# Kernel optimization log

Measured on AMD Instinct MI355X. Metric: run time of the kernel, lower is better.

Reference implementation:

```python
import jax, jax.numpy as jnp
import numpy as np

GRID_SIZE = 16
NUM_VOXELS = GRID_SIZE ** 3


def setup_inputs() -> dict:
    key = jax.random.key(0)
    k1, k2, k3 = jax.random.split(key, 3)
    B, D, N = 4, 128, 100000
    features = jax.random.normal(k1, (B, D, N), dtype=jnp.float32)
    xyz_normalized = jax.random.uniform(k2, (B, N, 3), dtype=jnp.float32)
    mask = jax.random.randint(k3, (B, N), 0, 2, dtype=jnp.int32)
    return {"features": features, "xyz_normalized": xyz_normalized, "mask": mask}


def _flat_voxel_idx(xyz):
    # xyz: [B, N, 3] in [0,1); voxel index per point, flattened z*G*G + y*G + x
    G = GRID_SIZE
    vi = jnp.clip((xyz * G).astype(jnp.int32), 0, G - 1)  # [B, N, 3]
    return vi[..., 2] * (G * G) + vi[..., 1] * G + vi[..., 0]  # [B, N]


def reference(features, xyz_normalized, mask):
    # features: [B, D, N], xyz_normalized: [B, N, 3], mask: [B, N] int (0/1)
    idx = _flat_voxel_idx(xyz_normalized)  # [B, N]
    feats = features * mask[:, None, :].astype(features.dtype)  # [B, D, N]

    def per_batch(f_dn, idx_n, m_n):
        # scatter-add features: segment_sum over points -> [V, D] -> [D, V]
        sums = jax.ops.segment_sum(f_dn.T, idx_n, num_segments=NUM_VOXELS)  # [V, D]
        counts = jax.ops.segment_sum(m_n, idx_n, num_segments=NUM_VOXELS)  # [V]
        counts = jnp.maximum(counts, 1).astype(f_dn.dtype)
        return (sums / counts[:, None]).T  # [D, V]

    return jax.vmap(per_batch)(feats, idx, mask)  # [B, D, V]
```

## Files before the change

kernel.cpp:

```cpp
#include <hip/hip_runtime.h>

#define GSZ  16
#define NVOX 4096
#define BB   4
#define DD   128

__global__ void k_voxidx(const float* __restrict__ xyz, const int* __restrict__ mask,
                         unsigned short* __restrict__ idxm, int* __restrict__ counts,
                         int N) {
    int n = blockIdx.x * blockDim.x + threadIdx.x;
    int b = blockIdx.y;
    if (n >= N) return;
    size_t i = (size_t)b * N + n;
    float x = xyz[3 * i + 0];
    float y = xyz[3 * i + 1];
    float z = xyz[3 * i + 2];
    int vx = min(max((int)(x * (float)GSZ), 0), GSZ - 1);
    int vy = min(max((int)(y * (float)GSZ), 0), GSZ - 1);
    int vz = min(max((int)(z * (float)GSZ), 0), GSZ - 1);
    int idx = vz * GSZ * GSZ + vy * GSZ + vx;
    if (mask[i] != 0) {
        idxm[i] = (unsigned short)idx;
        atomicAdd(&counts[b * NVOX + idx], 1);
    } else {
        idxm[i] = 0xFFFFu;
    }
}

__global__ __launch_bounds__(1024, 8) void k_scatter(const float* __restrict__ feats,
                                                     const unsigned short* __restrict__ idxm,
                                                     const int* __restrict__ counts,
                                                     float* __restrict__ out, int N) {
    __shared__ float acc[NVOX];
    int d = blockIdx.x & (DD - 1);
    int b = blockIdx.x >> 7;

    for (int j = threadIdx.x; j < NVOX; j += 1024) acc[j] = 0.f;
    __syncthreads();

    const float*          f  = feats + ((size_t)b * DD + (size_t)d) * (size_t)N;
    const unsigned short* ib = idxm + (size_t)b * N;

    const int stride = 1024 * 8;
    const int nmain  = (N / stride) * stride;
    const int niter  = nmain / stride;
    const int t8     = (int)threadIdx.x * 8;

#define PROC(id, val)                                        \
    {                                                        \
        unsigned int _i = (id);                              \
        if (_i != 0xFFFFu) atomicAdd(&acc[_i], (val));       \
    }

    if (niter > 0) {
        uint4  iv = *reinterpret_cast<const uint4*>(ib + t8);
        float4 r0 = *reinterpret_cast<const float4*>(f + t8);
        float4 r1 = *reinterpret_cast<const float4*>(f + t8 + 4);
        for (int it = 0; it < niter; it++) {
            int inext = (it + 1 < niter) ? (it + 1) * stride + t8 : t8;
            uint4  ivn = *reinterpret_cast<const uint4*>(ib + inext);
            float4 r0n = *reinterpret_cast<const float4*>(f + inext);
            float4 r1n = *reinterpret_cast<const float4*>(f + inext + 4);

            PROC(iv.x & 0xFFFFu, r0.x)
            PROC(iv.x >> 16,     r0.y)
            PROC(iv.y & 0xFFFFu, r0.z)
            PROC(iv.y >> 16,     r0.w)
            PROC(iv.z & 0xFFFFu, r1.x)
            PROC(iv.z >> 16,     r1.y)
            PROC(iv.w & 0xFFFFu, r1.z)
            PROC(iv.w >> 16,     r1.w)

            iv = ivn; r0 = r0n; r1 = r1n;
        }
    }
    for (int p = nmain + (int)threadIdx.x; p < N; p += 1024) {
        unsigned int id = ib[p];
        if (id != 0xFFFFu) atomicAdd(&acc[id], f[p]);
    }
#undef PROC

    __syncthreads();

    const int* cb = counts + b * NVOX;
    float*     ob = out + ((size_t)b * DD + (size_t)d) * (size_t)NVOX;
    {
        int j = threadIdx.x;
        float4 a = reinterpret_cast<float4*>(acc)[j];
        int4   c = reinterpret_cast<const int4*>(cb)[j];
        a.x /= (float)max(c.x, 1);
        a.y /= (float)max(c.y, 1);
        a.z /= (float)max(c.z, 1);
        a.w /= (float)max(c.w, 1);
        reinterpret_cast<float4*>(ob)[j] = a;
    }
}

extern "C" void kernel_launch(void* const* d_in, const int* in_sizes, int n_in,
                              void* d_out, int out_size, void* d_ws, size_t ws_size,
                              hipStream_t stream) {
    const float* feats = (const float*)d_in[0];
    const float* xyz   = (const float*)d_in[1];
    const int*   mask  = (const int*)d_in[2];
    float*       out   = (float*)d_out;

    int N = in_sizes[2] / BB;

    int*            counts = (int*)d_ws;
    unsigned short* idxm   = (unsigned short*)((char*)d_ws +
                                               (size_t)BB * NVOX * sizeof(int));

    hipMemsetAsync(counts, 0, (size_t)BB * NVOX * sizeof(int), stream);

    k_voxidx<<<dim3((N + 255) / 256, BB), 256, 0, stream>>>(xyz, mask, idxm, counts, N);

    k_scatter<<<BB * DD, 1024, 0, stream>>>(feats, idxm, counts, out, N);
}
```

Measured before the change: 350.4 us.

## Compact masked points before scatter to skip masked-out work

Adds a stream-compaction pipeline: the voxel-index pass packs each point's position and voxel id into one 32-bit word and counts valid points per tile, a scan kernel computes tile offsets, and a compact kernel writes only unmasked entries. The scatter kernel then iterates only over valid points, gathering features by index instead of streaming all features contiguously. This is meant to halve the atomics and the loop trip count, at the cost of extra kernels and uncoalesced gathers of the feature rows. The gather still pulls whole cache lines, so feature bandwidth may not shrink much.

```diff
diff --git a/kernel.cpp b/kernel.cpp
--- a/kernel.cpp
+++ b/kernel.cpp
@@ -4,31 +4,139 @@
 #define NVOX 4096
 #define BB   4
 #define DD   128
-
-__global__ void k_voxidx(const float* __restrict__ xyz, const int* __restrict__ mask,
-                         unsigned short* __restrict__ idxm, int* __restrict__ counts,
-                         int N) {
-    int n = blockIdx.x * blockDim.x + threadIdx.x;
-    int b = blockIdx.y;
-    if (n >= N) return;
-    size_t i = (size_t)b * N + n;
-    float x = xyz[3 * i + 0];
-    float y = xyz[3 * i + 1];
-    float z = xyz[3 * i + 2];
-    int vx = min(max((int)(x * (float)GSZ), 0), GSZ - 1);
-    int vy = min(max((int)(y * (float)GSZ), 0), GSZ - 1);
-    int vz = min(max((int)(z * (float)GSZ), 0), GSZ - 1);
-    int idx = vz * GSZ * GSZ + vy * GSZ + vx;
-    if (mask[i] != 0) {
-        idxm[i] = (unsigned short)idx;
-        atomicAdd(&counts[b * NVOX + idx], 1);
+#define TPB1 256
+#define TILE 2048
+#define PPT  8
+
+__global__ __launch_bounds__(TPB1) void k_voxidx(const float* __restrict__ xyz,
+                                                 const int* __restrict__ mask,
+                                                 unsigned int* __restrict__ pack,
+                                                 int* __restrict__ counts,
+                                                 int* __restrict__ bcount,
+                                                 int N, int NB) {
+    int tile = blockIdx.x, b = blockIdx.y;
+    __shared__ int s_cnt;
+    if (threadIdx.x == 0) s_cnt = 0;
+    __syncthreads();
+
+    const float*  xb = xyz  + (size_t)b * N * 3;
+    const int*    mb = mask + (size_t)b * N;
+    unsigned int* pb = pack + (size_t)b * N;
+    int*          cb = counts + b * NVOX;
+
+    int p0 = tile * TILE + (int)threadIdx.x * PPT;
+    int cnt = 0;
+
+    if (p0 + PPT <= N) {
+        float a[3 * PPT];
+        float4* av = (float4*)a;
+        const float4* xv = (const float4*)(xb + 3 * (size_t)p0);
+#pragma unroll
+        for (int q = 0; q < 6; q++) av[q] = xv[q];
+        const int4* mv = (const int4*)(mb + p0);
+        int4 mA = mv[0], mB = mv[1];
+        int mk[PPT] = {mA.x, mA.y, mA.z, mA.w, mB.x, mB.y, mB.z, mB.w};
+        unsigned int pk[PPT];
+#pragma unroll
+        for (int k = 0; k < PPT; k++) {
+            int vx = min(max((int)(a[3 * k + 0] * (float)GSZ), 0), GSZ - 1);
+            int vy = min(max((int)(a[3 * k + 1] * (float)GSZ), 0), GSZ - 1);
+            int vz = min(max((int)(a[3 * k + 2] * (float)GSZ), 0), GSZ - 1);
+            int idx = vz * GSZ * GSZ + vy * GSZ + vx;
+            if (mk[k] != 0) {
+                pk[k] = ((unsigned int)(p0 + k) << 12) | (unsigned int)idx;
+                cnt++;
+                atomicAdd(&cb[idx], 1);
+            } else {
+                pk[k] = 0xFFFFFFFFu;
+            }
+        }
+        uint4* pv = (uint4*)(pb + p0);
+        pv[0] = make_uint4(pk[0], pk[1], pk[2], pk[3]);
+        pv[1] = make_uint4(pk[4], pk[5], pk[6], pk[7]);
     } else {
-        idxm[i] = 0xFFFFu;
+        for (int k = 0; k < PPT; k++) {
+            int p = p0 + k;
+            if (p >= N) break;
+            float x = xb[3 * (size_t)p + 0];
+            float y = xb[3 * (size_t)p + 1];
+            float z = xb[3 * (size_t)p + 2];
+            int vx = min(max((int)(x * (float)GSZ), 0), GSZ - 1);
+            int vy = min(max((int)(y * (float)GSZ), 0), GSZ - 1);
+            int vz = min(max((int)(z * (float)GSZ), 0), GSZ - 1);
+            int idx = vz * GSZ * GSZ + vy * GSZ + vx;
+            if (mb[p] != 0) {
+                pb[p] = ((unsigned int)p << 12) | (unsigned int)idx;
+                cnt++;
+                atomicAdd(&cb[idx], 1);
+            } else {
+                pb[p] = 0xFFFFFFFFu;
+            }
+        }
+    }
+    atomicAdd(&s_cnt, cnt);
+    __syncthreads();
+    if (threadIdx.x == 0) bcount[b * NB + tile] = s_cnt;
+}
+
+__global__ void k_scan(const int* __restrict__ bcount, int* __restrict__ boff,
+                       int* __restrict__ M, int NB) {
+    int b = threadIdx.x;
+    if (b < BB) {
+        int run = 0;
+        for (int j = 0; j < NB; j++) {
+            boff[b * NB + j] = run;
+            run += bcount[b * NB + j];
+        }
+        M[b] = run;
+    }
+}
+
+__global__ __launch_bounds__(TPB1) void k_compact(const unsigned int* __restrict__ pack,
+                                                  const int* __restrict__ boff,
+                                                  unsigned int* __restrict__ comp,
+                                                  int N, int NB) {
+    int tile = blockIdx.x, b = blockIdx.y;
+    const unsigned int* pb = pack + (size_t)b * N;
+    unsigned int*       ob = comp + (size_t)b * N;
+
+    int p0 = tile * TILE + (int)threadIdx.x * PPT;
+    unsigned int pk[PPT];
+#pragma unroll
+    for (int k = 0; k < PPT; k++) pk[k] = 0xFFFFFFFFu;
+
+    if (p0 + PPT <= N) {
+        const uint4* pv = (const uint4*)(pb + p0);
+        uint4 A = pv[0], Bq = pv[1];
+        pk[0] = A.x;  pk[1] = A.y;  pk[2] = A.z;  pk[3] = A.w;
+        pk[4] = Bq.x; pk[5] = Bq.y; pk[6] = Bq.z; pk[7] = Bq.w;
+    } else {
+        for (int k = 0; k < PPT; k++)
+            if (p0 + k < N) pk[k] = pb[p0 + k];
+    }
+    int cnt = 0;
+#pragma unroll
+    for (int k = 0; k < PPT; k++) cnt += (pk[k] != 0xFFFFFFFFu) ? 1 : 0;
+
+    __shared__ int s[TPB1];
+    s[threadIdx.x] = cnt;
+    __syncthreads();
+    for (int off = 1; off < TPB1; off <<= 1) {
+        int v = (threadIdx.x >= (unsigned)off) ? s[threadIdx.x - off] : 0;
+        __syncthreads();
+        s[threadIdx.x] += v;
+        __syncthreads();
+    }
+    int pos = boff[b * NB + tile] + s[threadIdx.x] - cnt;
+#pragma unroll
+    for (int k = 0; k < PPT; k++) {
+        if (pk[k] != 0xFFFFFFFFu) ob[pos++] = pk[k];
     }
 }
 
 __global__ __launch_bounds__(1024, 8) void k_scatter(const float* __restrict__ feats,
-                                                     const unsigned short* __restrict__ idxm,
+                                                     const unsigned int* __restrict__ comp,
+                                                     const int* __restrict__ M,
                                                      const int* __restrict__ counts,
                                                      float* __restrict__ out, int N) {
     __shared__ float acc[NVOX];
@@ -38,48 +146,35 @@
     for (int j = threadIdx.x; j < NVOX; j += 1024) acc[j] = 0.f;
     __syncthreads();
 
-    const float*          f  = feats + ((size_t)b * DD + (size_t)d) * (size_t)N;
-    const unsigned short* ib = idxm + (size_t)b * N;
-
-    const int stride = 1024 * 8;
-    const int nmain  = (N / stride) * stride;
-    const int niter  = nmain / stride;
-    const int t8     = (int)threadIdx.x * 8;
-
-#define PROC(id, val)                                        \
-    {                                                        \
-        unsigned int _i = (id);                              \
-        if (_i != 0xFFFFu) atomicAdd(&acc[_i], (val));       \
-    }
+    int Mb = M[b];
+    const float*        f  = feats + ((size_t)b * DD + (size_t)d) * (size_t)N;
+    const unsigned int* cp = comp + (size_t)b * N;
+
+    const int stride = 1024 * 4;
+    int niter = Mb / stride;
+    int nmain = niter * stride;
+    int t4 = (int)threadIdx.x * 4;
 
     if (niter > 0) {
-        uint4  iv = *reinterpret_cast<const uint4*>(ib + t8);
-        float4 r0 = *reinterpret_cast<const float4*>(f + t8);
-        float4 r1 = *reinterpret_cast<const float4*>(f + t8 + 4);
+        uint4 e = *reinterpret_cast<const uint4*>(cp + t4);
         for (int it = 0; it < niter; it++) {
-            int inext = (it + 1 < niter) ? (it + 1) * stride + t8 : t8;
-            uint4  ivn = *reinterpret_cast<const uint4*>(ib + inext);
-            float4 r0n = *reinterpret_cast<const float4*>(f + inext);
-            float4 r1n = *reinterpret_cast<const float4*>(f + inext + 4);
-
-            PROC(iv.x & 0xFFFFu, r0.x)
-            PROC(iv.x >> 16,     r0.y)
-            PROC(iv.y & 0xFFFFu, r0.z)
-            PROC(iv.y >> 16,     r0.w)
-            PROC(iv.z & 0xFFFFu, r1.x)
-            PROC(iv.z >> 16,     r1.y)
-            PROC(iv.w & 0xFFFFu, r1.z)
-            PROC(iv.w >> 16,     r1.w)
-
-            iv = ivn; r0 = r0n; r1 = r1n;
-        }
-    }
-    for (int p = nmain + (int)threadIdx.x; p < N; p += 1024) {
-        unsigned int id = ib[p];
-        if (id != 0xFFFFu) atomicAdd(&acc[id], f[p]);
-    }
-#undef PROC
-
+            int inext = (it + 1 < niter) ? (it + 1) * stride + t4 : t4;
+            uint4 en = *reinterpret_cast<const uint4*>(cp + inext);
+            float v0 = f[e.x >> 12];
+            float v1 = f[e.y >> 12];
+            float v2 = f[e.z >> 12];
+            float v3 = f[e.w >> 12];
+            atomicAdd(&acc[e.x & 0xFFFu], v0);
+            atomicAdd(&acc[e.y & 0xFFFu], v1);
+            atomicAdd(&acc[e.z & 0xFFFu], v2);
+            atomicAdd(&acc[e.w & 0xFFFu], v3);
+            e = en;
+        }
+    }
+    for (int p = nmain + (int)threadIdx.x; p < Mb; p += 1024) {
+        unsigned int ee = cp[p];
+        atomicAdd(&acc[ee & 0xFFFu], f[ee >> 12]);
+    }
     __syncthreads();
 
     const int* cb = counts + b * NVOX;
@@ -104,15 +199,21 @@
     const int*   mask  = (const int*)d_in[2];
     float*       out   = (float*)d_out;
 
-    int N = in_sizes[2] / BB;
-
-    int*            counts = (int*)d_ws;
-    unsigned short* idxm   = (unsigned short*)((char*)d_ws +
-                                               (size_t)BB * NVOX * sizeof(int));
+    int N  = in_sizes[2] / BB;
+    int NB = (N + TILE - 1) / TILE;
+
+    char* w = (char*)d_ws;
+    int*          counts = (int*)w;                       w += (size_t)BB * NVOX * sizeof(int);
+    int*          bcount = (int*)w;                       w += ((size_t)BB * NB * sizeof(int) + 255) & ~255ull;
+    int*          boff   = (int*)w;                       w += ((size_t)BB * NB * sizeof(int) + 255) & ~255ull;
+    int*          Mcnt   = (int*)w;                       w += 256;
+    unsigned int* pack   = (unsigned int*)w;              w += (size_t)BB * N * sizeof(unsigned int);
+    unsigned int* comp   = (unsigned int*)w;
 
     hipMemsetAsync(counts, 0, (size_t)BB * NVOX * sizeof(int), stream);
 
-    k_voxidx<<<dim3((N + 255) / 256, BB), 256, 0, stream>>>(xyz, mask, idxm, counts, N);
-
-    k_scatter<<<BB * DD, 1024, 0, stream>>>(feats, idxm, counts, out, N);
-}
+    k_voxidx <<<dim3(NB, BB), TPB1, 0, stream>>>(xyz, mask, pack, counts, bcount, N, NB);
+    k_scan   <<<1, 64, 0, stream>>>(bcount, boff, Mcnt, NB);
+    k_compact<<<dim3(NB, BB), TPB1, 0, stream>>>(pack, boff, comp, N, NB);
+    k_scatter<<<BB * DD, 1024, 0, stream>>>(feats, comp, Mcnt, counts, out, N);
+}
```

After: 361.9 us. 1.03x slower.

## Accumulate two channels per LDS atomic using packed fp16 adds, per-tile histograms

Applied to the files above, without the earlier changes.

The scatter kernel now handles two feature channels per block. Both values for a point are packed into one fp16x2 and added with a single ds_pk_add_f16 LDS atomic, which halves the number of shared-memory atomics and blocks. The global count atomics and the memset are replaced by per-tile LDS histograms written out as ushort, and the scatter kernel reduces them. The prep kernel now handles 16 points per thread with vectorized loads. The cost is that voxel sums are accumulated in fp16, which loses accuracy and may exceed tolerance.

```diff
diff --git a/kernel.cpp b/kernel.cpp
--- a/kernel.cpp
+++ b/kernel.cpp
@@ -1,99 +1,172 @@
 #include <hip/hip_runtime.h>
 
-#define GSZ  16
-#define NVOX 4096
-#define BB   4
-#define DD   128
+#define GSZ   16
+#define NVOX  4096
+#define BB    4
+#define DD    128
+#define PThr  256
+#define PPT   16
+#define PTILE (PThr * PPT)
 
-__global__ void k_voxidx(const float* __restrict__ xyz, const int* __restrict__ mask,
-                         unsigned short* __restrict__ idxm, int* __restrict__ counts,
-                         int N) {
-    int n = blockIdx.x * blockDim.x + threadIdx.x;
-    int b = blockIdx.y;
-    if (n >= N) return;
-    size_t i = (size_t)b * N + n;
-    float x = xyz[3 * i + 0];
-    float y = xyz[3 * i + 1];
-    float z = xyz[3 * i + 2];
-    int vx = min(max((int)(x * (float)GSZ), 0), GSZ - 1);
-    int vy = min(max((int)(y * (float)GSZ), 0), GSZ - 1);
-    int vz = min(max((int)(z * (float)GSZ), 0), GSZ - 1);
-    int idx = vz * GSZ * GSZ + vy * GSZ + vx;
-    if (mask[i] != 0) {
-        idxm[i] = (unsigned short)idx;
-        atomicAdd(&counts[b * NVOX + idx], 1);
-    } else {
-        idxm[i] = 0xFFFFu;
-    }
+typedef __fp16 half2v __attribute__((ext_vector_type(2)));
+
+__device__ __forceinline__ void lds_pk_add_f16(unsigned byte_off, float va, float vb) {
+    half2v h = __builtin_amdgcn_cvt_pkrtz(va, vb);
+    unsigned hv;
+    __builtin_memcpy(&hv, &h, 4);
+    asm volatile("ds_pk_add_f16 %0, %1" : : "v"(byte_off), "v"(hv) : "memory");
 }
 
-__global__ __launch_bounds__(1024, 8) void k_scatter(const float* __restrict__ feats,
-                                                     const unsigned short* __restrict__ idxm,
-                                                     const int* __restrict__ counts,
-                                                     float* __restrict__ out, int N) {
-    __shared__ float acc[NVOX];
-    int d = blockIdx.x & (DD - 1);
-    int b = blockIdx.x >> 7;
-
-    for (int j = threadIdx.x; j < NVOX; j += 1024) acc[j] = 0.f;
+__global__ __launch_bounds__(PThr) void k_prep(const float* __restrict__ xyz,
+                                               const int* __restrict__ mask,
+                                               unsigned short* __restrict__ idxm,
+                                               unsigned short* __restrict__ histg,
+                                               int N, int NT) {
+    __shared__ unsigned int hist[NVOX];
+    const int tile = blockIdx.x, b = blockIdx.y;
+    for (int j = threadIdx.x; j < NVOX; j += PThr) hist[j] = 0u;
     __syncthreads();
 
-    const float*          f  = feats + ((size_t)b * DD + (size_t)d) * (size_t)N;
+    const float*    xb = xyz  + (size_t)b * N * 3;
+    const int*      mb = mask + (size_t)b * N;
+    unsigned short* ib = idxm + (size_t)b * N;
+
+    const int p0 = tile * PTILE + (int)threadIdx.x * PPT;
+
+    if (p0 + PPT <= N) {
+        float a[3 * PPT];
+        float4* av = (float4*)a;
+        const float4* xv = (const float4*)(xb + 3 * (size_t)p0);
+#pragma unroll
+        for (int q = 0; q < 12; q++) av[q] = xv[q];
+        int mk[PPT];
+        const int4* mv = (const int4*)(mb + p0);
+#pragma unroll
+        for (int q = 0; q < 4; q++) {
+            int4 m4 = mv[q];
+            mk[4*q+0] = m4.x; mk[4*q+1] = m4.y; mk[4*q+2] = m4.z; mk[4*q+3] = m4.w;
+        }
+        alignas(16) unsigned short pk[PPT];
+#pragma unroll
+        for (int k = 0; k < PPT; k++) {
+            int vx = min(max((int)(a[3*k+0] * (float)GSZ), 0), GSZ - 1);
+            int vy = min(max((int)(a[3*k+1] * (float)GSZ), 0), GSZ - 1);
+            int vz = min(max((int)(a[3*k+2] * (float)GSZ), 0), GSZ - 1);
+            int idx = vz * GSZ * GSZ + vy * GSZ + vx;
+            if (mk[k] != 0) {
+                pk[k] = (unsigned short)idx;
+                atomicAdd(&hist[idx], 1u);
+            } else {
+                pk[k] = 0xFFFFu;
+            }
+        }
+        uint4* dst = (uint4*)(ib + p0);
+        dst[0] = ((const uint4*)pk)[0];
+        dst[1] = ((const uint4*)pk)[1];
+    } else {
+        for (int k = 0; k < PPT; k++) {
+            int p = p0 + k;
+            if (p >= N) break;
+            float x = xb[3*(size_t)p+0], y = xb[3*(size_t)p+1], z = xb[3*(size_t)p+2];
+            int vx = min(max((int)(x * (float)GSZ), 0), GSZ - 1);
+            int vy = min(max((int)(y * (float)GSZ), 0), GSZ - 1);
+            int vz = min(max((int)(z * (float)GSZ), 0), GSZ - 1);
+            int idx = vz * GSZ * GSZ + vy * GSZ + vx;
+            if (mb[p] != 0) { ib[p] = (unsigned short)idx; atomicAdd(&hist[idx], 1u); }
+            else            { ib[p] = 0xFFFFu; }
+        }
+    }
+    __syncthreads();
+    unsigned short* hg = histg + ((size_t)b * NT + tile) * NVOX;
+    for (int j = threadIdx.x; j < NVOX; j += PThr) hg[j] = (unsigned short)hist[j];
+}
+
+__global__ __launch_bounds__(1024) void k_scatter(const float* __restrict__ feats,
+                                                  const unsigned short* __restrict__ idxm,
+                                                  const unsigned short* __restrict__ histg,
+                                                  float* __restrict__ out, int N, int NT) {
+    __shared__ half2v acc[NVOX];
+    const int dp = blockIdx.x & 63;
+    const int b  = blockIdx.x >> 6;
+    const int d0 = dp * 2;
+
+    {
+        half2v z = { (__fp16)0.f, (__fp16)0.f };
+        for (int j = threadIdx.x; j < NVOX; j += 1024) acc[j] = z;
+    }
+    __syncthreads();
+
     const unsigned short* ib = idxm + (size_t)b * N;
+    const float* f0 = feats + ((size_t)b * DD + (size_t)d0) * (size_t)N;
+    const float* f1 = f0 + N;
+    const unsigned accbase = (unsigned)(size_t)(void*)&acc[0];
+
+#define PROC(idx_, va_, vb_)                                       \
+    {                                                              \
+        unsigned _i = (idx_);                                      \
+        if (_i != 0xFFFFu) lds_pk_add_f16(accbase + _i * 4u, (va_), (vb_)); \
+    }
 
     const int stride = 1024 * 8;
-    const int nmain  = (N / stride) * stride;
-    const int niter  = nmain / stride;
+    const int niter  = N / stride;
     const int t8     = (int)threadIdx.x * 8;
 
-#define PROC(id, val)                                        \
-    {                                                        \
-        unsigned int _i = (id);                              \
-        if (_i != 0xFFFFu) atomicAdd(&acc[_i], (val));       \
-    }
-
     if (niter > 0) {
-        uint4  iv = *reinterpret_cast<const uint4*>(ib + t8);
-        float4 r0 = *reinterpret_cast<const float4*>(f + t8);
-        float4 r1 = *reinterpret_cast<const float4*>(f + t8 + 4);
+        uint4  iv = *(const uint4*)(ib + t8);
+        float4 a0 = *(const float4*)(f0 + t8);
+        float4 a1 = *(const float4*)(f0 + t8 + 4);
+        float4 b0 = *(const float4*)(f1 + t8);
+        float4 b1 = *(const float4*)(f1 + t8 + 4);
         for (int it = 0; it < niter; it++) {
             int inext = (it + 1 < niter) ? (it + 1) * stride + t8 : t8;
-            uint4  ivn = *reinterpret_cast<const uint4*>(ib + inext);
-            float4 r0n = *reinterpret_cast<const float4*>(f + inext);
-            float4 r1n = *reinterpret_cast<const float4*>(f + inext + 4);
+            uint4  ivn = *(const uint4*)(ib + inext);
+            float4 a0n = *(const float4*)(f0 + inext);
+            float4 a1n = *(const float4*)(f0 + inext + 4);
+            float4 b0n = *(const float4*)(f1 + inext);
+            float4 b1n = *(const float4*)(f1 + inext + 4);
 
-            PROC(iv.x & 0xFFFFu, r0.x)
-            PROC(iv.x >> 16,     r0.y)
-            PROC(iv.y & 0xFFFFu, r0.z)
-            PROC(iv.y >> 16,     r0.w)
-            PROC(iv.z & 0xFFFFu, r1.x)
-            PROC(iv.z >> 16,     r1.y)
-            PROC(iv.w & 0xFFFFu, r1.z)
-            PROC(iv.w >> 16,     r1.w)
+            PROC(iv.x & 0xFFFFu, a0.x, b0.x)
+            PROC(iv.x >> 16,     a0.y, b0.y)
+            PROC(iv.y & 0xFFFFu, a0.z, b0.z)
+            PROC(iv.y >> 16,     a0.w, b0.w)
+            PROC(iv.z & 0xFFFFu, a1.x, b1.x)
+            PROC(iv.z >> 16,     a1.y, b1.y)
+            PROC(iv.w & 0xFFFFu, a1.z, b1.z)
+            PROC(iv.w >> 16,     a1.w, b1.w)
 
-            iv = ivn; r0 = r0n; r1 = r1n;
+            iv = ivn; a0 = a0n; a1 = a1n; b0 = b0n; b1 = b1n;
         }
     }
-    for (int p = nmain + (int)threadIdx.x; p < N; p += 1024) {
-        unsigned int id = ib[p];
-        if (id != 0xFFFFu) atomicAdd(&acc[id], f[p]);
+    for (int p = niter * stride + (int)threadIdx.x; p < N; p += 1024) {
+        unsigned id = ib[p];
+        if (id != 0xFFFFu) lds_pk_add_f16(accbase + id * 4u, f0[p], f1[p]);
     }
 #undef PROC
 
+    const int v0 = (int)threadIdx.x * 4;
+    int c0 = 0, c1 = 0, c2 = 0, c3 = 0;
+    {
+        const unsigned short* hb = histg + (size_t)b * NT * NVOX + v0;
+        for (int t = 0; t < NT; t++) {
+            ushort4 h = *(const ushort4*)(hb + (size_t)t * NVOX);
+            c0 += h.x; c1 += h.y; c2 += h.z; c3 += h.w;
+        }
+    }
     __syncthreads();
 
-    const int* cb = counts + b * NVOX;
-    float*     ob = out + ((size_t)b * DD + (size_t)d) * (size_t)NVOX;
-    {
-        int j = threadIdx.x;
-        float4 a = reinterpret_cast<float4*>(acc)[j];
-        int4   c = reinterpret_cast<const int4*>(cb)[j];
-        a.x /= (float)max(c.x, 1);
-        a.y /= (float)max(c.y, 1);
-        a.z /= (float)max(c.z, 1);
-        a.w /= (float)max(c.w, 1);
-        reinterpret_cast<float4*>(ob)[j] = a;
-    }
+    half2v s0 = acc[v0+0], s1 = acc[v0+1], s2 = acc[v0+2], s3 = acc[v0+3];
+    float i0 = 1.f / (float)max(c0, 1);
+    float i1 = 1.f / (float)max(c1, 1);
+    float i2 = 1.f / (float)max(c2, 1);
+    float i3 = 1.f / (float)max(c3, 1);
+    float4 oa, ob;
+    oa.x = (float)s0.x * i0;  ob.x = (float)s0.y * i0;
+    oa.y = (float)s1.x * i1;  ob.y = (float)s1.y * i1;
+    oa.z = (float)s2.x * i2;  ob.z = (float)s2.y * i2;
+    oa.w = (float)s3.x * i3;  ob.w = (float)s3.y * i3;
+    float* r0 = out + ((size_t)b * DD + (size_t)d0) * (size_t)NVOX + v0;
+    *(float4*)r0          = oa;
+    *(float4*)(r0 + NVOX) = ob;
 }
 
 extern "C" void kernel_launch(void* const* d_in, const int* in_sizes, int n_in,
@@ -104,15 +177,14 @@
     const int*   mask  = (const int*)d_in[2];
     float*       out   = (float*)d_out;
 
-    int N = in_sizes[2] / BB;
+    int N  = in_sizes[2] / BB;
+    int NT = (N + PTILE - 1) / PTILE;
 
-    int*            counts = (int*)d_ws;
-    unsigned short* idxm   = (unsigned short*)((char*)d_ws +
-                                               (size_t)BB * NVOX * sizeof(int));
+    char* w = (char*)d_ws;
+    unsigned short* idxm  = (unsigned short*)w;
+    w += (((size_t)BB * N * sizeof(unsigned short)) + 255) & ~(size_t)255;
+    unsigned short* histg = (unsigned short*)w;
 
-    hipMemsetAsync(counts, 0, (size_t)BB * NVOX * sizeof(int), stream);
-
-    k_voxidx<<<dim3((N + 255) / 256, BB), 256, 0, stream>>>(xyz, mask, idxm, counts, N);
-
-    k_scatter<<<BB * DD, 1024, 0, stream>>>(feats, idxm, counts, out, N);
+    k_prep   <<<dim3(NT, BB), PThr, 0, stream>>>(xyz, mask, idxm, histg, N, NT);
+    k_scatter<<<BB * (DD / 2), 1024, 0, stream>>>(feats, idxm, histg, out, N, NT);
 }
```

Measured after the change: 300.3 us. 1.17x faster.
